# Kernel tuning notes

Measured on AMD Instinct MI355X. Metric: run time of the kernel, lower is better.

Reference implementation:

```python
import jax, jax.numpy as jnp
import numpy as np
import math

V, D, H, L, T, B = 32000, 768, 12, 4, 1024, 2
HD = D // H  # head size 64
EMB_SCALE = math.sqrt(D)  # DynamicTanh path
EPS = 1e-5


def setup_inputs() -> dict:
    key = jax.random.key(0)
    ks = jax.random.split(key, 10)
    def rn(k, shape, std=0.02):
        return jax.random.normal(k, shape, jnp.float32) * std
    return {
        "idx": jax.random.randint(ks[0], (B, T), 0, V, dtype=jnp.int32).astype(jnp.int64) if False else jax.random.randint(ks[0], (B, T), 0, V),
        "wte": rn(ks[1], (V, D)),            # tied with lm_head
        "wpe": rn(ks[2], (T, D)),            # block_size == T
        "ln1_alpha": jnp.full((L, 1), 0.5, jnp.float32),
        "ln1_w": jnp.ones((L, D), jnp.float32),
        "ln1_b": jnp.zeros((L, D), jnp.float32),
        "wq": rn(ks[3], (L, D, D)),          # stored [in,out] (torch W.T)
        "wk": rn(ks[4], (L, D, D)),
        "wv": rn(ks[5], (L, D, D)),
        "wo": rn(ks[6], (L, D, D)),
        "bo": jnp.zeros((L, D), jnp.float32),
        "ln2_alpha": jnp.full((L, 1), 0.5, jnp.float32),
        "ln2_w": jnp.ones((L, D), jnp.float32),
        "ln2_b": jnp.zeros((L, D), jnp.float32),
        "w_fc": rn(ks[7], (L, D, 4 * D)),
        "b_fc": jnp.zeros((L, 4 * D), jnp.float32),
        "w_proj": rn(ks[8], (L, 4 * D, D), std=0.02 / math.sqrt(2 * L)),
        "b_proj": jnp.zeros((L, D), jnp.float32),
        "lnf_alpha": jnp.full((1,), 0.5, jnp.float32),
        "lnf_w": jnp.ones((D,), jnp.float32),
        "lnf_b": jnp.zeros((D,), jnp.float32),
    }


def _dyt(x, alpha, w, b):
    # DynamicTanh: layernorm-style normalize, then w * tanh(alpha * xn) + b
    mu = x.mean(-1, keepdims=True)
    var = ((x - mu) ** 2).mean(-1, keepdims=True)
    xn = (x - mu) * jax.lax.rsqrt(var + EPS)
    return w * jnp.tanh(alpha * xn) + b


def reference(idx, wte, wpe, ln1_alpha, ln1_w, ln1_b, wq, wk, wv, wo, bo,
              ln2_alpha, ln2_w, ln2_b, w_fc, b_fc, w_proj, b_proj,
              lnf_alpha, lnf_w, lnf_b):
    Bb, Tt = idx.shape
    x = (wte[idx] + wpe[:Tt][None]) * EMB_SCALE          # [B,T,D]; dropout = eval identity
    mask = jnp.tril(jnp.ones((Tt, Tt), bool))
    scale = 1.0 / math.sqrt(HD)
    for l in range(L):
        h = _dyt(x, ln1_alpha[l], ln1_w[l], ln1_b[l])
        q = (h @ wq[l]).reshape(Bb, Tt, H, HD)
        k = (h @ wk[l]).reshape(Bb, Tt, H, HD)
        v = (h @ wv[l]).reshape(Bb, Tt, H, HD)
        att = jnp.einsum('bqhd,bkhd->bhqk', q, k) * scale
        att = jnp.where(mask, att, -jnp.inf)
        att = jax.nn.softmax(att, axis=-1)
        o = jnp.einsum('bhqk,bkhd->bqhd', att, v).reshape(Bb, Tt, D)
        x = x + o @ wo[l] + bo[l]
        h = _dyt(x, ln2_alpha[l], ln2_w[l], ln2_b[l])
        h = jax.nn.gelu(h @ w_fc[l] + b_fc[l], approximate=False)  # torch nn.GELU = exact erf
        x = x + h @ w_proj[l] + b_proj[l]
    x = _dyt(x, lnf_alpha, lnf_w, lnf_b)
    return x @ wte.T                                     # tied lm_head, [B,T,V]
```

## Files before the change

### kernel.cpp

```cpp
#include <hip/hip_runtime.h>
#include <hip/hip_bf16.h>
#include <math.h>

constexpr int B_ = 2, T_ = 1024, D_ = 768, H_ = 12, L_ = 4, V_ = 32000;
constexpr int M_ = B_ * T_;
constexpr int FF_ = 4 * D_;
constexpr int QKVN_ = 3 * D_;
#define EMB_SCALE 27.712812921102035f
#define EPS_ 1e-5f

typedef __attribute__((ext_vector_type(8))) short short8_t;
typedef __attribute__((ext_vector_type(4))) float float4_t;

__device__ __forceinline__ float bf2f(__hip_bfloat16 v) { return __bfloat162float(v); }
__device__ __forceinline__ __hip_bfloat16 f2bf(float v) { return __float2bfloat16(v); }

__device__ __forceinline__ void gl_lds16(const __hip_bfloat16* g, __hip_bfloat16* l) {
    __builtin_amdgcn_global_load_lds(
        (const __attribute__((address_space(1))) void*)g,
        (__attribute__((address_space(3))) void*)l, 16, 0, 0);
}

__global__ __launch_bounds__(256) void convert_kernel(
    const float* __restrict__ src, __hip_bfloat16* __restrict__ dst, size_t n)
{
    size_t i = ((size_t)blockIdx.x * 256 + threadIdx.x) * 4;
    if (i + 3 < n) {
        float4 f = *(const float4*)(src + i);
        dst[i + 0] = f2bf(f.x);
        dst[i + 1] = f2bf(f.y);
        dst[i + 2] = f2bf(f.z);
        dst[i + 3] = f2bf(f.w);
    }
}

__global__ __launch_bounds__(256) void tconv_kernel(
    const float* __restrict__ src, __hip_bfloat16* __restrict__ dst,
    int K, int N, size_t sstride, size_t dstride)
{
    __shared__ float tile[32][33];
    const float* S = src + (size_t)blockIdx.z * sstride;
    __hip_bfloat16* Dd = dst + (size_t)blockIdx.z * dstride;
    int n0 = blockIdx.x * 32, k0 = blockIdx.y * 32;
    int tx = threadIdx.x & 31, ty = threadIdx.x >> 5;
#pragma unroll
    for (int i = 0; i < 32; i += 8)
        tile[ty + i][tx] = S[(size_t)(k0 + ty + i) * N + n0 + tx];
    __syncthreads();
#pragma unroll
    for (int i = 0; i < 32; i += 8)
        Dd[(size_t)(n0 + ty + i) * K + k0 + tx] = f2bf(tile[tx][ty + i]);
}

__global__ __launch_bounds__(256) void embed_kernel(
    const int* __restrict__ idx, const float* __restrict__ wte,
    const float* __restrict__ wpe, float* __restrict__ x)
{
    int row = blockIdx.x, tid = threadIdx.x;
    int t = row & (T_ - 1);
    int tok = idx[row];
#pragma unroll
    for (int i = 0; i < 3; ++i) {
        int c = i * 256 + tid;
        x[(size_t)row * D_ + c] =
            (wte[(size_t)tok * D_ + c] + wpe[(size_t)t * D_ + c]) * EMB_SCALE;
    }
}

__global__ __launch_bounds__(256) void dyt_kernel(
    const float* __restrict__ x, __hip_bfloat16* __restrict__ h,
    const float* __restrict__ w, const float* __restrict__ bb,
    const float* __restrict__ alpha_p)
{
    const int row = blockIdx.x, tid = threadIdx.x;
    const float* xr = x + (size_t)row * D_;
    float v[3];
    float s = 0.f, ss = 0.f;
#pragma unroll
    for (int i = 0; i < 3; ++i) {
        v[i] = xr[i * 256 + tid];
        s += v[i];
        ss += v[i] * v[i];
    }
#pragma unroll
    for (int off = 32; off >= 1; off >>= 1) {
        s  += __shfl_xor(s,  off, 64);
        ss += __shfl_xor(ss, off, 64);
    }
    __shared__ float sh[8];
    int wave = tid >> 6;
    if ((tid & 63) == 0) { sh[wave] = s; sh[wave + 4] = ss; }
    __syncthreads();
    s  = sh[0] + sh[1] + sh[2] + sh[3];
    ss = sh[4] + sh[5] + sh[6] + sh[7];
    float mu = s * (1.f / D_);
    float var = ss * (1.f / D_) - mu * mu;
    float rstd = rsqrtf(var + EPS_);
    float alpha = *alpha_p;
#pragma unroll
    for (int i = 0; i < 3; ++i) {
        int c = i * 256 + tid;
        float xn = (v[i] - mu) * rstd;
        h[(size_t)row * D_ + c] = f2bf(w[c] * tanhf(alpha * xn) + bb[c]);
    }
}

constexpr int LSTR = 72;

__global__ __launch_bounds__(256) void fattn_kernel(
    const __hip_bfloat16* __restrict__ qkv, __hip_bfloat16* __restrict__ o)
{
    const int qt = gridDim.x - 1 - blockIdx.x;
    const int hh = blockIdx.y, b = blockIdx.z;
    const int q0 = qt * 64;
    const int tid = threadIdx.x;
    const int wave = tid >> 6, lane = tid & 63;
    const int quad = lane >> 4, l16 = lane & 15;
    const size_t rs = QKVN_;

    __shared__ __hip_bfloat16 Ks[64 * LSTR];
    __shared__ __hip_bfloat16 Vts[64 * LSTR];
    __shared__ __hip_bfloat16 Ps[4][16 * LSTR];

    const __hip_bfloat16* qrow = qkv + (size_t)(b * T_ + q0 + wave * 16 + l16) * rs + hh * 64;
    short8_t qf0 = *(const short8_t*)(qrow + quad * 8);
    short8_t qf1 = *(const short8_t*)(qrow + 32 + quad * 8);

    float4_t Oacc[4];
#pragma unroll
    for (int j = 0; j < 4; ++j) Oacc[j] = (float4_t){0.f, 0.f, 0.f, 0.f};
    float mrow[4], lrow[4];
#pragma unroll
    for (int r = 0; r < 4; ++r) { mrow[r] = -1e30f; lrow[r] = 0.f; }

    const __hip_bfloat16* kbase = qkv + (size_t)b * T_ * rs + D_ + hh * 64;
    const __hip_bfloat16* vbase = qkv + (size_t)b * T_ * rs + 2 * D_ + hh * 64;

    const int sr = tid >> 2;
    const int sc = (tid & 3) * 8;
    const int vr = lane;
    const int vc0 = wave * 16;

    for (int kt = 0; kt <= qt; ++kt) {
        const int kt0 = kt * 64;
        uint4 kv0 = *(const uint4*)(kbase + (size_t)(kt0 + sr) * rs + sc);
        uint4 kv1 = *(const uint4*)(kbase + (size_t)(kt0 + sr) * rs + sc + 32);
        uint4 vv0 = *(const uint4*)(vbase + (size_t)(kt0 + vr) * rs + vc0);
        uint4 vv1 = *(const uint4*)(vbase + (size_t)(kt0 + vr) * rs + vc0 + 8);
        __syncthreads();
        *(uint4*)(Ks + sr * LSTR + sc)      = kv0;
        *(uint4*)(Ks + sr * LSTR + sc + 32) = kv1;
        {
            const __hip_bfloat16* vp = (const __hip_bfloat16*)&vv0;
#pragma unroll
            for (int i = 0; i < 8; ++i) Vts[(vc0 + i) * LSTR + vr] = vp[i];
            vp = (const __hip_bfloat16*)&vv1;
#pragma unroll
            for (int i = 0; i < 8; ++i) Vts[(vc0 + 8 + i) * LSTR + vr] = vp[i];
        }
        __syncthreads();

        float4_t S[4];
#pragma unroll
        for (int jt = 0; jt < 4; ++jt) {
            short8_t kf0 = *(const short8_t*)(Ks + (jt * 16 + l16) * LSTR + quad * 8);
            short8_t kf1 = *(const short8_t*)(Ks + (jt * 16 + l16) * LSTR + 32 + quad * 8);
            float4_t s = (float4_t){0.f, 0.f, 0.f, 0.f};
            s = __builtin_amdgcn_mfma_f32_16x16x32_bf16(qf0, kf0, s, 0, 0, 0);
            s = __builtin_amdgcn_mfma_f32_16x16x32_bf16(qf1, kf1, s, 0, 0, 0);
            S[jt] = s;
        }

        if (kt == qt) {
#pragma unroll
            for (int jt = 0; jt < 4; ++jt)
#pragma unroll
                for (int r = 0; r < 4; ++r) {
                    int qg = wave * 16 + quad * 4 + r;
                    int kg = jt * 16 + l16;
                    S[jt][r] = (kg > qg) ? -1e30f : S[jt][r] * 0.125f;
                }
        } else {
#pragma unroll
            for (int jt = 0; jt < 4; ++jt)
#pragma unroll
                for (int r = 0; r < 4; ++r) S[jt][r] *= 0.125f;
        }

        float mnew[4], alphav[4];
#pragma unroll
        for (int r = 0; r < 4; ++r) {
            float mx = fmaxf(fmaxf(S[0][r], S[1][r]), fmaxf(S[2][r], S[3][r]));
            mx = fmaxf(mx, __shfl_xor(mx, 1, 64));
            mx = fmaxf(mx, __shfl_xor(mx, 2, 64));
            mx = fmaxf(mx, __shfl_xor(mx, 4, 64));
            mx = fmaxf(mx, __shfl_xor(mx, 8, 64));
            mnew[r] = fmaxf(mrow[r], mx);
            alphav[r] = __expf(mrow[r] - mnew[r]);
            mrow[r] = mnew[r];
        }
        float psum[4] = {0.f, 0.f, 0.f, 0.f};
#pragma unroll
        for (int jt = 0; jt < 4; ++jt)
#pragma unroll
            for (int r = 0; r < 4; ++r) {
                float p = __expf(S[jt][r] - mnew[r]);
                S[jt][r] = p;
                psum[r] += p;
            }
#pragma unroll
        for (int r = 0; r < 4; ++r) {
            float ps = psum[r];
            ps += __shfl_xor(ps, 1, 64);
            ps += __shfl_xor(ps, 2, 64);
            ps += __shfl_xor(ps, 4, 64);
            ps += __shfl_xor(ps, 8, 64);
            lrow[r] = lrow[r] * alphav[r] + ps;
        }

        __hip_bfloat16* ps_base = Ps[wave];
#pragma unroll
        for (int jt = 0; jt < 4; ++jt)
#pragma unroll
            for (int r = 0; r < 4; ++r)
                ps_base[(quad * 4 + r) * LSTR + jt * 16 + l16] = f2bf(S[jt][r]);

#pragma unroll
        for (int j = 0; j < 4; ++j)
#pragma unroll
            for (int r = 0; r < 4; ++r) Oacc[j][r] *= alphav[r];

        short8_t pf0 = *(const short8_t*)(ps_base + l16 * LSTR + quad * 8);
        short8_t pf1 = *(const short8_t*)(ps_base + l16 * LSTR + 32 + quad * 8);
#pragma unroll
        for (int j = 0; j < 4; ++j) {
            short8_t vf0 = *(const short8_t*)(Vts + (j * 16 + l16) * LSTR + quad * 8);
            short8_t vf1 = *(const short8_t*)(Vts + (j * 16 + l16) * LSTR + 32 + quad * 8);
            Oacc[j] = __builtin_amdgcn_mfma_f32_16x16x32_bf16(pf0, vf0, Oacc[j], 0, 0, 0);
            Oacc[j] = __builtin_amdgcn_mfma_f32_16x16x32_bf16(pf1, vf1, Oacc[j], 0, 0, 0);
        }
    }

    float inv_l[4];
#pragma unroll
    for (int r = 0; r < 4; ++r) inv_l[r] = 1.f / lrow[r];
    __hip_bfloat16* orow = o + (size_t)(b * T_ + q0 + wave * 16) * D_ + hh * 64;
#pragma unroll
    for (int j = 0; j < 4; ++j)
#pragma unroll
        for (int r = 0; r < 4; ++r)
            orow[(size_t)(quad * 4 + r) * D_ + j * 16 + l16] = f2bf(Oacc[j][r] * inv_l[r]);
}

__device__ __forceinline__ float gelu_exact(float t) {
    return 0.5f * t * (1.0f + erff(t * 0.70710678118654752f));
}

template <int EPI>
__global__ __launch_bounds__(256, 2) void gemm_btp(
    const __hip_bfloat16* __restrict__ A, const __hip_bfloat16* __restrict__ Bt,
    float* __restrict__ outF, __hip_bfloat16* __restrict__ outB,
    const float* __restrict__ bias, const float* __restrict__ res,
    int M, int N, int K)
{
    __shared__ __hip_bfloat16 lds[4 * 8192];
    const int tid = threadIdx.x;
    const int wave = tid >> 6, lane = tid & 63;
    const int quad = lane >> 4, l16 = lane & 15;
    const int m0 = blockIdx.y * 128, n0 = blockIdx.x * 128;
    const int wm = (wave >> 1) * 64, wn = (wave & 1) * 64;
    const int NT = K >> 5;

    const int srow = tid >> 2;
    const int sq   = (tid & 3) ^ ((srow >> 1) & 3);
    const __hip_bfloat16* gA = A  + (size_t)(m0 + srow) * K + sq * 8;
    const __hip_bfloat16* gB = Bt + (size_t)(n0 + srow) * K + sq * 8;
    char* ldsc = (char*)lds;
    const int wb = wave * 1024;

#define STGP(tt) do {                                                      \
        const size_t ko = (size_t)(tt) * 32;                               \
        char* bb = ldsc + ((tt) & 3) * 16384 + wb;                         \
        gl_lds16(gA + ko,                  (__hip_bfloat16*)(bb));         \
        gl_lds16(gA + (size_t)64 * K + ko, (__hip_bfloat16*)(bb + 4096));  \
        gl_lds16(gB + ko,                  (__hip_bfloat16*)(bb + 8192));  \
        gl_lds16(gB + (size_t)64 * K + ko, (__hip_bfloat16*)(bb + 12288)); \
    } while (0)

    const int xe = (quad ^ ((l16 >> 1) & 3)) * 16;

    float4_t acc[4][4];
#pragma unroll
    for (int i = 0; i < 4; ++i)
#pragma unroll
        for (int j = 0; j < 4; ++j) acc[i][j] = (float4_t){0.f, 0.f, 0.f, 0.f};

    STGP(0); STGP(1); STGP(2);
    asm volatile("s_waitcnt vmcnt(8)" ::: "memory");
    __builtin_amdgcn_sched_barrier(0);
    __builtin_amdgcn_s_barrier();

    for (int t = 0; t < NT; ++t) {
        if (t + 3 < NT) STGP(t + 3);
        const char* base = ldsc + (t & 3) * 16384;
        short8_t af[4], bfv[4];
#pragma unroll
        for (int i = 0; i < 4; ++i)
            af[i]  = *(const short8_t*)(base + (wm + i * 16 + l16) * 64 + xe);
#pragma unroll
        for (int j = 0; j < 4; ++j)
            bfv[j] = *(const short8_t*)(base + 8192 + (wn + j * 16 + l16) * 64 + xe);
        asm volatile("s_waitcnt lgkmcnt(0)" ::: "memory");
        __builtin_amdgcn_sched_barrier(0);
        __builtin_amdgcn_s_setprio(1);
#pragma unroll
        for (int i = 0; i < 4; ++i)
#pragma unroll
            for (int j = 0; j < 4; ++j)
                acc[i][j] = __builtin_amdgcn_mfma_f32_16x16x32_bf16(
                    af[i], bfv[j], acc[i][j], 0, 0, 0);
        __builtin_amdgcn_s_setprio(0);
        if (t + 3 < NT) {
            asm volatile("s_waitcnt vmcnt(8)" ::: "memory");
        } else if (t + 2 < NT) {
            asm volatile("s_waitcnt vmcnt(4)" ::: "memory");
        } else if (t + 1 < NT) {
            asm volatile("s_waitcnt vmcnt(0)" ::: "memory");
        }
        __builtin_amdgcn_sched_barrier(0);
        __builtin_amdgcn_s_barrier();
    }
#undef STGP

#pragma unroll
    for (int i = 0; i < 4; ++i) {
#pragma unroll
        for (int j = 0; j < 4; ++j) {
            int colg = n0 + wn + j * 16 + l16;
#pragma unroll
            for (int rg = 0; rg < 4; ++rg) {
                int rowg = m0 + wm + i * 16 + quad * 4 + rg;
                size_t offo = (size_t)rowg * N + colg;
                float v = acc[i][j][rg];
                if (EPI == 0) {
                    outB[offo] = f2bf(v);
                } else if (EPI == 1) {
                    outF[offo] = res[offo] + v + bias[colg];
                } else if (EPI == 2) {
                    outB[offo] = f2bf(gelu_exact(v + bias[colg]));
                } else {
                    outF[offo] = v;
                }
            }
        }
    }
}

__global__ __launch_bounds__(512, 2) void gemm_lmhead(
    const __hip_bfloat16* __restrict__ A, const __hip_bfloat16* __restrict__ Bt,
    float* __restrict__ out)
{
    constexpr int K = D_;
    constexpr int N = V_;
    constexpr int NT = K / 32;
    __shared__ __hip_bfloat16 lds[32768];

    const int tid  = threadIdx.x;
    const int wave = tid >> 6, lane = tid & 63;
    const int quad = lane >> 4, l16 = lane & 15;

    const int flat = blockIdx.x;
    const int g = (flat & 7) * 125 + (flat >> 3);
    const int m0 = (g & 7) * 256, n0 = (g >> 3) * 256;

    const int wm = (wave >> 2) * 128;
    const int wn = (wave & 3) * 64;

    const int slr  = tid >> 2;
    const int sq   = (tid & 3) ^ ((slr >> 1) & 3);
    const int rbase = ((slr & 64) << 1) | (slr & 63);
    const __hip_bfloat16* gA = A  + (size_t)(m0 + rbase) * K + sq * 8;
    const __hip_bfloat16* gB = Bt + (size_t)(n0 + rbase) * K + sq * 8;
    const int wb = wave * 1024;
    char* ldsc = (char*)lds;

#define STG(gp, Xoff, hh, tt) \
    gl_lds16((gp) + (size_t)(hh) * 64 * K + (tt) * 32, \
             (__hip_bfloat16*)(ldsc + (((tt) & 1) * 32768 + (Xoff) + (hh) * 8192 + wb)))

    const int xe   = (quad ^ ((l16 >> 1) & 3)) * 16;
    const int aoff = wm * 32 + l16 * 64 + xe;
    const int boff = 16384 + ((wn >> 6) & 1) * 8192 + (wn & 128) * 32 + l16 * 64 + xe;

    float4_t acc[8][4];
#pragma unroll
    for (int i = 0; i < 8; ++i)
#pragma unroll
        for (int j = 0; j < 4; ++j) acc[i][j] = (float4_t){0.f, 0.f, 0.f, 0.f};

    STG(gA, 0,     0, 0); STG(gB, 16384, 0, 0);
    STG(gA, 0,     1, 0); STG(gB, 16384, 1, 0);
    STG(gA, 0,     0, 1); STG(gB, 16384, 0, 1);
    asm volatile("s_waitcnt vmcnt(2)" ::: "memory");
    __builtin_amdgcn_sched_barrier(0);
    __builtin_amdgcn_s_barrier();

    auto do_tile = [&](int tt, bool last2) {
        const char* base = ldsc + (tt & 1) * 32768;
        short8_t af[4], bf[4];
#pragma unroll
        for (int ii = 0; ii < 4; ++ii)
            af[ii] = *(const short8_t*)(base + ii * 1024 + aoff);
#pragma unroll
        for (int j = 0; j < 4; ++j)
            bf[j] = *(const short8_t*)(base + j * 1024 + boff);
        if (tt + 1 < NT) { STG(gA, 0, 1, tt + 1); STG(gB, 16384, 1, tt + 1); }
        __builtin_amdgcn_s_barrier();
        asm volatile("s_waitcnt lgkmcnt(0)" ::: "memory");
        __builtin_amdgcn_sched_barrier(0);
        __builtin_amdgcn_s_setprio(1);
#pragma unroll
        for (int ii = 0; ii < 4; ++ii)
#pragma unroll
            for (int j = 0; j < 4; ++j)
                acc[ii][j] = __builtin_amdgcn_mfma_f32_16x16x32_bf16(
                    af[ii], bf[j], acc[ii][j], 0, 0, 0);
        __builtin_amdgcn_s_setprio(0);
        __builtin_amdgcn_s_barrier();
#pragma unroll
        for (int ii = 0; ii < 4; ++ii)
            af[ii] = *(const short8_t*)(base + 8192 + ii * 1024 + aoff);
        if (tt + 2 < NT) { STG(gA, 0, 0, tt + 2); STG(gB, 16384, 0, tt + 2); }
        __builtin_amdgcn_s_barrier();
        asm volatile("s_waitcnt lgkmcnt(0)" ::: "memory");
        __builtin_amdgcn_sched_barrier(0);
        __builtin_amdgcn_s_setprio(1);
#pragma unroll
        for (int ii = 0; ii < 4; ++ii)
#pragma unroll
            for (int j = 0; j < 4; ++j)
                acc[4 + ii][j] = __builtin_amdgcn_mfma_f32_16x16x32_bf16(
                    af[ii], bf[j], acc[4 + ii][j], 0, 0, 0);
        __builtin_amdgcn_s_setprio(0);
        if (last2) {
            asm volatile("s_waitcnt vmcnt(0)" ::: "memory");
        } else {
            asm volatile("s_waitcnt vmcnt(2)" ::: "memory");
        }
        __builtin_amdgcn_sched_barrier(0);
        __builtin_amdgcn_s_barrier();
    };

    for (int t = 0; t + 2 < NT; t += 2) { do_tile(t, false); do_tile(t + 1, false); }
    do_tile(NT - 2, true);
    do_tile(NT - 1, false);
#undef STG

    float* orow = out + (size_t)(m0 + wm + quad * 4) * N + (n0 + wn + l16);
#pragma unroll
    for (int i = 0; i < 8; ++i)
#pragma unroll
        for (int j = 0; j < 4; ++j)
#pragma unroll
            for (int rg = 0; rg < 4; ++rg)
                orow[(size_t)(i * 16 + rg) * N + j * 16] = acc[i][j][rg];
}

extern "C" void kernel_launch(void* const* d_in, const int* in_sizes, int n_in,
                              void* d_out, int out_size, void* d_ws, size_t ws_size,
                              hipStream_t stream)
{
    const int*   idx   = (const int*)d_in[0];
    const float* wte   = (const float*)d_in[1];
    const float* wpe   = (const float*)d_in[2];
    const float* ln1_a = (const float*)d_in[3];
    const float* ln1_w = (const float*)d_in[4];
    const float* ln1_b = (const float*)d_in[5];
    const float* wq    = (const float*)d_in[6];
    const float* wk    = (const float*)d_in[7];
    const float* wv    = (const float*)d_in[8];
    const float* wo    = (const float*)d_in[9];
    const float* bo    = (const float*)d_in[10];
    const float* ln2_a = (const float*)d_in[11];
    const float* ln2_w = (const float*)d_in[12];
    const float* ln2_b = (const float*)d_in[13];
    const float* w_fc  = (const float*)d_in[14];
    const float* b_fc  = (const float*)d_in[15];
    const float* w_pr  = (const float*)d_in[16];
    const float* b_pr  = (const float*)d_in[17];
    const float* lnf_a = (const float*)d_in[18];
    const float* lnf_w = (const float*)d_in[19];
    const float* lnf_b = (const float*)d_in[20];
    float* out = (float*)d_out;

    char* ws = (char*)d_ws;
    size_t off = 0;
    auto alloc = [&](size_t bytes) -> char* {
        char* p = ws + off;
        off += (bytes + 255) & ~(size_t)255;
        return p;
    };
    __hip_bfloat16* wqkv_t = (__hip_bfloat16*)alloc((size_t)L_ * QKVN_ * D_ * 2);
    __hip_bfloat16* wo_t   = (__hip_bfloat16*)alloc((size_t)L_ * D_ * D_ * 2);
    __hip_bfloat16* wfc_t  = (__hip_bfloat16*)alloc((size_t)L_ * FF_ * D_ * 2);
    __hip_bfloat16* wpr_t  = (__hip_bfloat16*)alloc((size_t)L_ * D_ * FF_ * 2);
    __hip_bfloat16* wte_b  = (__hip_bfloat16*)alloc((size_t)V_ * D_ * 2);
    float*          x      = (float*)alloc((size_t)M_ * D_ * 4);
    __hip_bfloat16* h      = (__hip_bfloat16*)alloc((size_t)M_ * D_ * 2);
    __hip_bfloat16* qkv    = (__hip_bfloat16*)alloc((size_t)M_ * QKVN_ * 2);
    __hip_bfloat16* attno  = (__hip_bfloat16*)alloc((size_t)M_ * D_ * 2);
    __hip_bfloat16* mid    = (__hip_bfloat16*)alloc((size_t)M_ * FF_ * 2);
    (void)ws_size; (void)in_sizes; (void)n_in; (void)out_size;

    {
        size_t n = (size_t)V_ * D_;
        convert_kernel<<<dim3((unsigned)(n / 1024)), 256, 0, stream>>>(wte, wte_b, n);
    }
    size_t wstride = (size_t)D_ * D_;
    tconv_kernel<<<dim3(24, 24, L_), 256, 0, stream>>>(wq, wqkv_t + 0,            D_, D_, wstride, (size_t)QKVN_ * D_);
    tconv_kernel<<<dim3(24, 24, L_), 256, 0, stream>>>(wk, wqkv_t + (size_t)D_ * D_,   D_, D_, wstride, (size_t)QKVN_ * D_);
    tconv_kernel<<<dim3(24, 24, L_), 256, 0, stream>>>(wv, wqkv_t + (size_t)2 * D_ * D_, D_, D_, wstride, (size_t)QKVN_ * D_);
    tconv_kernel<<<dim3(24, 24, L_), 256, 0, stream>>>(wo, wo_t,                  D_, D_, wstride, wstride);
    tconv_kernel<<<dim3(96, 24, L_), 256, 0, stream>>>(w_fc, wfc_t, D_, FF_, (size_t)D_ * FF_, (size_t)FF_ * D_);
    tconv_kernel<<<dim3(24, 96, L_), 256, 0, stream>>>(w_pr, wpr_t, FF_, D_, (size_t)FF_ * D_, (size_t)D_ * FF_);

    embed_kernel<<<dim3(M_), 256, 0, stream>>>(idx, wte, wpe, x);

    for (int l = 0; l < L_; ++l) {
        dyt_kernel<<<dim3(M_), 256, 0, stream>>>(x, h, ln1_w + l * D_, ln1_b + l * D_, ln1_a + l);
        gemm_btp<0><<<dim3(QKVN_ / 128, M_ / 128), 256, 0, stream>>>(
            h, wqkv_t + (size_t)l * QKVN_ * D_, nullptr, qkv, nullptr, nullptr, M_, QKVN_, D_);
        fattn_kernel<<<dim3(T_ / 64, H_, B_), 256, 0, stream>>>(qkv, attno);
        gemm_btp<1><<<dim3(D_ / 128, M_ / 128), 256, 0, stream>>>(
            attno, wo_t + (size_t)l * D_ * D_, x, nullptr, bo + l * D_, x, M_, D_, D_);
        dyt_kernel<<<dim3(M_), 256, 0, stream>>>(x, h, ln2_w + l * D_, ln2_b + l * D_, ln2_a + l);
        gemm_btp<2><<<dim3(FF_ / 128, M_ / 128), 256, 0, stream>>>(
            h, wfc_t + (size_t)l * FF_ * D_, nullptr, mid, b_fc + l * FF_, nullptr, M_, FF_, D_);
        gemm_btp<1><<<dim3(D_ / 128, M_ / 128), 256, 0, stream>>>(
            mid, wpr_t + (size_t)l * D_ * FF_, x, nullptr, b_pr + l * D_, x, M_, D_, FF_);
    }

    dyt_kernel<<<dim3(M_), 256, 0, stream>>>(x, h, lnf_w, lnf_b, lnf_a);
    gemm_lmhead<<<dim3((M_ / 256) * (V_ / 256)), 512, 0, stream>>>(h, wte_b, out);
}
```

Baseline: 1.126 ms.

## Deepen lm-head GEMM pipeline to four stages and fuse small launches

The lm-head GEMM moves from a double-buffered, half-tile schedule to a four-stage LDS ring (128 KB). It prefetches three K-tiles ahead and keeps one barrier per tile, aiming to hide global-load latency and cut barrier overhead. Separately, the four Q/K/V/O weight transposes are merged into one launch, and the embedding is fused into the first DynamicTanh kernel to drop a launch and a re-read of x. The larger LDS footprint may limit occupancy to one block per CU, despite launch bounds requesting two.

```diff
diff --git a/kernel.cpp b/kernel.cpp
--- a/kernel.cpp
+++ b/kernel.cpp
@@ -52,35 +52,59 @@
         Dd[(size_t)(n0 + ty + i) * K + k0 + tx] = f2bf(tile[tx][ty + i]);
 }
 
-__global__ __launch_bounds__(256) void embed_kernel(
+__global__ __launch_bounds__(256) void tconv_qkvo_kernel(
+    const float* __restrict__ wq, const float* __restrict__ wk,
+    const float* __restrict__ wv, const float* __restrict__ wo,
+    __hip_bfloat16* __restrict__ wqkv_t, __hip_bfloat16* __restrict__ wo_t)
+{
+    __shared__ float tile[32][33];
+    const int z = blockIdx.z, l = z >> 2, which = z & 3;
+    const size_t dd = (size_t)D_ * D_;
+    const float* S = (which == 0 ? wq : which == 1 ? wk : which == 2 ? wv : wo) + (size_t)l * dd;
+    __hip_bfloat16* Dd = (which < 3) ? wqkv_t + (size_t)l * QKVN_ * D_ + (size_t)which * dd
+                                     : wo_t + (size_t)l * dd;
+    int n0 = blockIdx.x * 32, k0 = blockIdx.y * 32;
+    int tx = threadIdx.x & 31, ty = threadIdx.x >> 5;
+#pragma unroll
+    for (int i = 0; i < 32; i += 8)
+        tile[ty + i][tx] = S[(size_t)(k0 + ty + i) * D_ + n0 + tx];
+    __syncthreads();
+#pragma unroll
+    for (int i = 0; i < 32; i += 8)
+        Dd[(size_t)(n0 + ty + i) * D_ + k0 + tx] = f2bf(tile[tx][ty + i]);
+}
+
+template <bool EMBED>
+__global__ __launch_bounds__(256) void dyt_kernel(
+    const float* __restrict__ xin, float* __restrict__ xout,
+    __hip_bfloat16* __restrict__ h,
+    const float* __restrict__ w, const float* __restrict__ bb,
+    const float* __restrict__ alpha_p,
     const int* __restrict__ idx, const float* __restrict__ wte,
-    const float* __restrict__ wpe, float* __restrict__ x)
-{
-    int row = blockIdx.x, tid = threadIdx.x;
-    int t = row & (T_ - 1);
-    int tok = idx[row];
-#pragma unroll
-    for (int i = 0; i < 3; ++i) {
-        int c = i * 256 + tid;
-        x[(size_t)row * D_ + c] =
-            (wte[(size_t)tok * D_ + c] + wpe[(size_t)t * D_ + c]) * EMB_SCALE;
-    }
-}
-
-__global__ __launch_bounds__(256) void dyt_kernel(
-    const float* __restrict__ x, __hip_bfloat16* __restrict__ h,
-    const float* __restrict__ w, const float* __restrict__ bb,
-    const float* __restrict__ alpha_p)
+    const float* __restrict__ wpe)
 {
     const int row = blockIdx.x, tid = threadIdx.x;
-    const float* xr = x + (size_t)row * D_;
     float v[3];
     float s = 0.f, ss = 0.f;
-#pragma unroll
-    for (int i = 0; i < 3; ++i) {
-        v[i] = xr[i * 256 + tid];
-        s += v[i];
-        ss += v[i] * v[i];
+    if (EMBED) {
+        const int t = row & (T_ - 1);
+        const int tok = idx[row];
+#pragma unroll
+        for (int i = 0; i < 3; ++i) {
+            int c = i * 256 + tid;
+            v[i] = (wte[(size_t)tok * D_ + c] + wpe[(size_t)t * D_ + c]) * EMB_SCALE;
+            xout[(size_t)row * D_ + c] = v[i];
+            s += v[i];
+            ss += v[i] * v[i];
+        }
+    } else {
+        const float* xr = xin + (size_t)row * D_;
+#pragma unroll
+        for (int i = 0; i < 3; ++i) {
+            v[i] = xr[i * 256 + tid];
+            s += v[i];
+            ss += v[i] * v[i];
+        }
     }
 #pragma unroll
     for (int off = 32; off >= 1; off >>= 1) {
@@ -363,7 +387,7 @@
     constexpr int K = D_;
     constexpr int N = V_;
     constexpr int NT = K / 32;
-    __shared__ __hip_bfloat16 lds[32768];
+    __shared__ __hip_bfloat16 lds[4 * 16384];
 
     const int tid  = threadIdx.x;
     const int wave = tid >> 6, lane = tid & 63;
@@ -376,21 +400,23 @@
     const int wm = (wave >> 2) * 128;
     const int wn = (wave & 3) * 64;
 
-    const int slr  = tid >> 2;
-    const int sq   = (tid & 3) ^ ((slr >> 1) & 3);
-    const int rbase = ((slr & 64) << 1) | (slr & 63);
-    const __hip_bfloat16* gA = A  + (size_t)(m0 + rbase) * K + sq * 8;
-    const __hip_bfloat16* gB = Bt + (size_t)(n0 + rbase) * K + sq * 8;
+    const int srow = tid >> 2;
+    const int sq   = (tid & 3) ^ ((srow >> 1) & 3);
+    const __hip_bfloat16* gA = A  + (size_t)(m0 + srow) * K + sq * 8;
+    const __hip_bfloat16* gB = Bt + (size_t)(n0 + srow) * K + sq * 8;
+    char* ldsc = (char*)lds;
     const int wb = wave * 1024;
-    char* ldsc = (char*)lds;
-
-#define STG(gp, Xoff, hh, tt) \
-    gl_lds16((gp) + (size_t)(hh) * 64 * K + (tt) * 32, \
-             (__hip_bfloat16*)(ldsc + (((tt) & 1) * 32768 + (Xoff) + (hh) * 8192 + wb)))
-
-    const int xe   = (quad ^ ((l16 >> 1) & 3)) * 16;
-    const int aoff = wm * 32 + l16 * 64 + xe;
-    const int boff = 16384 + ((wn >> 6) & 1) * 8192 + (wn & 128) * 32 + l16 * 64 + xe;
+
+#define STGP(tt) do {                                                        \
+        const size_t ko = (size_t)(tt) * 32;                                 \
+        char* bb = ldsc + ((tt) & 3) * 32768 + wb;                           \
+        gl_lds16(gA + ko,                   (__hip_bfloat16*)(bb));          \
+        gl_lds16(gA + (size_t)128 * K + ko, (__hip_bfloat16*)(bb + 8192));   \
+        gl_lds16(gB + ko,                   (__hip_bfloat16*)(bb + 16384));  \
+        gl_lds16(gB + (size_t)128 * K + ko, (__hip_bfloat16*)(bb + 24576));  \
+    } while (0)
+
+    const int xe = (quad ^ ((l16 >> 1) & 3)) * 16;
 
     float4_t acc[8][4];
 #pragma unroll
@@ -398,63 +424,42 @@
 #pragma unroll
         for (int j = 0; j < 4; ++j) acc[i][j] = (float4_t){0.f, 0.f, 0.f, 0.f};
 
-    STG(gA, 0,     0, 0); STG(gB, 16384, 0, 0);
-    STG(gA, 0,     1, 0); STG(gB, 16384, 1, 0);
-    STG(gA, 0,     0, 1); STG(gB, 16384, 0, 1);
-    asm volatile("s_waitcnt vmcnt(2)" ::: "memory");
+    STGP(0); STGP(1); STGP(2);
+    asm volatile("s_waitcnt vmcnt(8)" ::: "memory");
     __builtin_amdgcn_sched_barrier(0);
     __builtin_amdgcn_s_barrier();
 
-    auto do_tile = [&](int tt, bool last2) {
-        const char* base = ldsc + (tt & 1) * 32768;
-        short8_t af[4], bf[4];
-#pragma unroll
-        for (int ii = 0; ii < 4; ++ii)
-            af[ii] = *(const short8_t*)(base + ii * 1024 + aoff);
+    for (int t = 0; t < NT; ++t) {
+        if (t + 3 < NT) STGP(t + 3);
+        const char* base = ldsc + (t & 3) * 32768;
+        short8_t af[8], bfv[4];
+#pragma unroll
+        for (int i = 0; i < 8; ++i)
+            af[i]  = *(const short8_t*)(base + (wm + i * 16 + l16) * 64 + xe);
 #pragma unroll
         for (int j = 0; j < 4; ++j)
-            bf[j] = *(const short8_t*)(base + j * 1024 + boff);
-        if (tt + 1 < NT) { STG(gA, 0, 1, tt + 1); STG(gB, 16384, 1, tt + 1); }
-        __builtin_amdgcn_s_barrier();
+            bfv[j] = *(const short8_t*)(base + 16384 + (wn + j * 16 + l16) * 64 + xe);
         asm volatile("s_waitcnt lgkmcnt(0)" ::: "memory");
         __builtin_amdgcn_sched_barrier(0);
         __builtin_amdgcn_s_setprio(1);
 #pragma unroll
-        for (int ii = 0; ii < 4; ++ii)
+        for (int i = 0; i < 8; ++i)
 #pragma unroll
             for (int j = 0; j < 4; ++j)
-                acc[ii][j] = __builtin_amdgcn_mfma_f32_16x16x32_bf16(
-                    af[ii], bf[j], acc[ii][j], 0, 0, 0);
+                acc[i][j] = __builtin_amdgcn_mfma_f32_16x16x32_bf16(
+                    af[i], bfv[j], acc[i][j], 0, 0, 0);
         __builtin_amdgcn_s_setprio(0);
-        __builtin_amdgcn_s_barrier();
-#pragma unroll
-        for (int ii = 0; ii < 4; ++ii)
-            af[ii] = *(const short8_t*)(base + 8192 + ii * 1024 + aoff);
-        if (tt + 2 < NT) { STG(gA, 0, 0, tt + 2); STG(gB, 16384, 0, tt + 2); }
-        __builtin_amdgcn_s_barrier();
-        asm volatile("s_waitcnt lgkmcnt(0)" ::: "memory");
-        __builtin_amdgcn_sched_barrier(0);
-        __builtin_amdgcn_s_setprio(1);
-#pragma unroll
-        for (int ii = 0; ii < 4; ++ii)
-#pragma unroll
-            for (int j = 0; j < 4; ++j)
-                acc[4 + ii][j] = __builtin_amdgcn_mfma_f32_16x16x32_bf16(
-                    af[ii], bf[j], acc[4 + ii][j], 0, 0, 0);
-        __builtin_amdgcn_s_setprio(0);
-        if (last2) {
+        if (t + 3 < NT) {
+            asm volatile("s_waitcnt vmcnt(8)" ::: "memory");
+        } else if (t + 2 < NT) {
+            asm volatile("s_waitcnt vmcnt(4)" ::: "memory");
+        } else if (t + 1 < NT) {
             asm volatile("s_waitcnt vmcnt(0)" ::: "memory");
-        } else {
-            asm volatile("s_waitcnt vmcnt(2)" ::: "memory");
         }
         __builtin_amdgcn_sched_barrier(0);
         __builtin_amdgcn_s_barrier();
-    };
-
-    for (int t = 0; t + 2 < NT; t += 2) { do_tile(t, false); do_tile(t + 1, false); }
-    do_tile(NT - 2, true);
-    do_tile(NT - 1, false);
-#undef STG
+    }
+#undef STGP
 
     float* orow = out + (size_t)(m0 + wm + quad * 4) * N + (n0 + wn + l16);
 #pragma unroll
@@ -516,30 +521,34 @@
         size_t n = (size_t)V_ * D_;
         convert_kernel<<<dim3((unsigned)(n / 1024)), 256, 0, stream>>>(wte, wte_b, n);
     }
-    size_t wstride = (size_t)D_ * D_;
-    tconv_kernel<<<dim3(24, 24, L_), 256, 0, stream>>>(wq, wqkv_t + 0,            D_, D_, wstride, (size_t)QKVN_ * D_);
-    tconv_kernel<<<dim3(24, 24, L_), 256, 0, stream>>>(wk, wqkv_t + (size_t)D_ * D_,   D_, D_, wstride, (size_t)QKVN_ * D_);
-    tconv_kernel<<<dim3(24, 24, L_), 256, 0, stream>>>(wv, wqkv_t + (size_t)2 * D_ * D_, D_, D_, wstride, (size_t)QKVN_ * D_);
-    tconv_kernel<<<dim3(24, 24, L_), 256, 0, stream>>>(wo, wo_t,                  D_, D_, wstride, wstride);
+    tconv_qkvo_kernel<<<dim3(24, 24, 4 * L_), 256, 0, stream>>>(
+        wq, wk, wv, wo, wqkv_t, wo_t);
     tconv_kernel<<<dim3(96, 24, L_), 256, 0, stream>>>(w_fc, wfc_t, D_, FF_, (size_t)D_ * FF_, (size_t)FF_ * D_);
     tconv_kernel<<<dim3(24, 96, L_), 256, 0, stream>>>(w_pr, wpr_t, FF_, D_, (size_t)FF_ * D_, (size_t)D_ * FF_);
 
-    embed_kernel<<<dim3(M_), 256, 0, stream>>>(idx, wte, wpe, x);
+    dyt_kernel<true><<<dim3(M_), 256, 0, stream>>>(
+        nullptr, x, h, ln1_w, ln1_b, ln1_a, idx, wte, wpe);
 
     for (int l = 0; l < L_; ++l) {
-        dyt_kernel<<<dim3(M_), 256, 0, stream>>>(x, h, ln1_w + l * D_, ln1_b + l * D_, ln1_a + l);
+        if (l > 0)
+            dyt_kernel<false><<<dim3(M_), 256, 0, stream>>>(
+                x, nullptr, h, ln1_w + l * D_, ln1_b + l * D_, ln1_a + l,
+                nullptr, nullptr, nullptr);
         gemm_btp<0><<<dim3(QKVN_ / 128, M_ / 128), 256, 0, stream>>>(
             h, wqkv_t + (size_t)l * QKVN_ * D_, nullptr, qkv, nullptr, nullptr, M_, QKVN_, D_);
         fattn_kernel<<<dim3(T_ / 64, H_, B_), 256, 0, stream>>>(qkv, attno);
         gemm_btp<1><<<dim3(D_ / 128, M_ / 128), 256, 0, stream>>>(
             attno, wo_t + (size_t)l * D_ * D_, x, nullptr, bo + l * D_, x, M_, D_, D_);
-        dyt_kernel<<<dim3(M_), 256, 0, stream>>>(x, h, ln2_w + l * D_, ln2_b + l * D_, ln2_a + l);
+        dyt_kernel<false><<<dim3(M_), 256, 0, stream>>>(
+            x, nullptr, h, ln2_w + l * D_, ln2_b + l * D_, ln2_a + l,
+            nullptr, nullptr, nullptr);
         gemm_btp<2><<<dim3(FF_ / 128, M_ / 128), 256, 0, stream>>>(
             h, wfc_t + (size_t)l * FF_ * D_, nullptr, mid, b_fc + l * FF_, nullptr, M_, FF_, D_);
         gemm_btp<1><<<dim3(D_ / 128, M_ / 128), 256, 0, stream>>>(
             mid, wpr_t + (size_t)l * D_ * FF_, x, nullptr, b_pr + l * D_, x, M_, D_, FF_);
     }
 
-    dyt_kernel<<<dim3(M_), 256, 0, stream>>>(x, h, lnf_w, lnf_b, lnf_a);
+    dyt_kernel<false><<<dim3(M_), 256, 0, stream>>>(
+        x, nullptr, h, lnf_w, lnf_b, lnf_a, nullptr, nullptr, nullptr);
     gemm_lmhead<<<dim3((M_ / 256) * (V_ / 256)), 512, 0, stream>>>(h, wte_b, out);
 }
```

After: 1.114 ms. About the same (-1.1%).
